# Kernel optimization log

Hardware: AMD Instinct MI355X
Metric: run time of the kernel (lower is better)

Reference implementation:

```python
import jax, jax.numpy as jnp
import numpy as np

B, T, D = 2, 4096, 1024
HD, HQ, KVH, W = 128, 8, 1, 1024   # head_dim, q_heads, kv_heads, window
HH, HG, K = 1536, 2048, 4          # hawk hidden, gmlp hidden, conv kernel
ALPHA_SCALE = float(np.log(8.0))   # alpha_log_scale (stored as log, used exp'd)


def setup_inputs() -> dict:
    key = jax.random.key(0)
    ks = jax.random.split(key, 16)
    n = lambda k, shape, std: jax.random.normal(k, shape, jnp.float32) * std
    return {
        'x': n(ks[0], (B, T, D), 1.0),
        'sn_g': jnp.ones((D,), jnp.float32),
        'q_w': n(ks[1], (HQ * HD, D), D ** -0.5),
        'kv_w': n(ks[2], (2 * KVH * HD, D), D ** -0.5),
        'ao_w': n(ks[3], (D, D), D ** -0.5),
        'sgn_g': jnp.ones((D,), jnp.float32),
        'sg_grow': n(ks[4], (2 * HG, D), D ** -0.5),
        'sg_shrink': n(ks[5], (D, HG), HG ** -0.5),
        'hn_g': jnp.ones((D,), jnp.float32),
        'h_in_w': n(ks[6], (2 * HH, D), D ** -0.5),
        'h_conv_w': n(ks[7], (HH, 1, K), K ** -0.5),
        'h_conv_b': jnp.zeros((HH,), jnp.float32),
        'h_gates_w': n(ks[8], (2 * HH, HH), HH ** -0.5),
        'h_gates_b': jnp.zeros((2 * HH,), jnp.float32),
        'h_forget': jnp.linspace(-4.323, -9.0, HH, dtype=jnp.float32),
        'h_out_w': n(ks[9], (D, HH), HH ** -0.5),
        'hgn_g': jnp.ones((D,), jnp.float32),
        'hg_grow': n(ks[10], (2 * HG, D), D ** -0.5),
        'hg_shrink': n(ks[11], (D, HG), HG ** -0.5),
    }


def rmsnorm(x, gamma):
    # original: gamma / dim**-0.5 * x / ||x||_2  (no eps)
    inv = jax.lax.rsqrt(jnp.sum(x * x, axis=-1, keepdims=True))
    return gamma * (x.shape[-1] ** 0.5) * x * inv


def rope(x, base=10000.0):
    # x: (B, T, H, HD); interleaved rotary over time axis 1
    t = x.shape[1]
    hd = x.shape[-1]
    inv = 1.0 / (base ** (jnp.arange(0, hd, 2, dtype=jnp.float32) / hd))
    ang = jnp.arange(t, dtype=jnp.float32)[:, None] * inv[None, :]  # (T, HD/2)
    cos = jnp.cos(ang)[None, :, None, :]
    sin = jnp.sin(ang)[None, :, None, :]
    x1, x2 = x[..., 0::2], x[..., 1::2]
    y1 = x1 * cos - x2 * sin
    y2 = x1 * sin + x2 * cos
    return jnp.stack([y1, y2], axis=-1).reshape(x.shape)


def sliding_mqa(x, q_w, kv_w, ao_w):
    # MQA with causal sliding window of W, computed in blocks of W
    q = (x @ q_w.T).reshape(B, T, HQ, HD)
    kv = (x @ kv_w.T).reshape(B, T, 2, KVH, HD)
    k = kv[:, :, 0, 0]  # (B, T, HD) since KVH == 1
    v = kv[:, :, 1, 0]
    q = rope(q)
    k = rope(k[:, :, None, :])[:, :, 0]
    nb = T // W
    qb = q.reshape(B, nb, W, HQ, HD)
    kb = k.reshape(B, nb, W, HD)
    vb = v.reshape(B, nb, W, HD)
    # prepend previous block (zeros for block 0)
    shift = lambda a: jnp.concatenate([jnp.zeros_like(a[:, :1]), a[:, :-1]], axis=1)
    k2 = jnp.concatenate([shift(kb), kb], axis=2)  # (B, nb, 2W, HD)
    v2 = jnp.concatenate([shift(vb), vb], axis=2)
    qi = jnp.arange(W)[:, None]
    kj = jnp.arange(2 * W)[None, :]
    base = (kj >= qi) & (kj <= qi + W)  # causal + window (i-j <= W)
    blk0 = base & (kj >= W)             # block 0 has no real previous block
    mask = jnp.where(jnp.arange(nb)[:, None, None] == 0, blk0[None], base[None])
    scores = jnp.einsum('bnqhd,bnkd->bhnqk', qb, k2) * (HD ** -0.5)
    scores = jnp.where(mask[None, None], scores, -jnp.inf)
    p = jax.nn.softmax(scores, axis=-1)
    o = jnp.einsum('bhnqk,bnkd->bnqhd', p, v2).reshape(B, T, HQ * HD)
    return o @ ao_w.T


def gated_mlp(x, grow_w, shrink_w):
    gate, h = jnp.split(x @ grow_w.T, 2, axis=-1)
    return (jax.nn.gelu(gate, approximate=False) * h) @ shrink_w.T


def hawk(x, in_w, conv_w, conv_b, gates_w, gates_b, forget_base, out_w):
    gate, u = jnp.split(x @ in_w.T, 2, axis=-1)  # (B, T, HH) each
    # depthwise causal conv1d (torch pads k-1 both sides then slices [:T])
    u_nch = jnp.transpose(u, (0, 2, 1))  # (B, HH, T)
    c = jax.lax.conv_general_dilated(
        u_nch, conv_w, window_strides=(1,), padding=[(K - 1, 0)],
        feature_group_count=HH, dimension_numbers=('NCH', 'OIH', 'NCH'))
    xc = jnp.transpose(c + conv_b[None, :, None], (0, 2, 1))  # (B, T, HH)
    fg, ig = jnp.split(xc @ gates_w.T + gates_b, 2, axis=-1)
    log_alpha = -np.exp(ALPHA_SCALE) * jax.nn.softplus(forget_base) * jax.nn.sigmoid(fg)
    alpha = jnp.exp(log_alpha)
    beta = jnp.sqrt(1.0 - alpha * alpha + 1e-6)
    xin = beta * jax.nn.sigmoid(ig) * xc
    # linear recurrence h_t = alpha_t * h_{t-1} + xin_t  via associative scan
    def combine(c1, c2):
        a1, x1 = c1
        a2, x2 = c2
        return a1 * a2, a2 * x1 + x2
    _, h = jax.lax.associative_scan(combine, (alpha, xin), axis=1)
    return (jax.nn.gelu(gate, approximate=False) * h) @ out_w.T


def reference(x, sn_g, q_w, kv_w, ao_w, sgn_g, sg_grow, sg_shrink,
              hn_g, h_in_w, h_conv_w, h_conv_b, h_gates_w, h_gates_b,
              h_forget, h_out_w, hgn_g, hg_grow, hg_shrink):
    x = x + sliding_mqa(rmsnorm(x, sn_g), q_w, kv_w, ao_w)
    x = x + gated_mlp(rmsnorm(x, sgn_g), sg_grow, sg_shrink)
    x = x + hawk(rmsnorm(x, hn_g), h_in_w, h_conv_w, h_conv_b,
                 h_gates_w, h_gates_b, h_forget, h_out_w)
    x = x + gated_mlp(rmsnorm(x, hgn_g), hg_grow, hg_shrink)
    return x
```

## Files before the change

### kernel.cpp

```cpp
#include <hip/hip_runtime.h>
#include <hip/hip_bf16.h>
#include <math.h>

#define B_  2
#define T_  4096
#define D_  1024
#define HD_ 128
#define HQ_ 8
#define W_  1024
#define HH_ 1536
#define HG_ 2048
#define KC_ 4

typedef float  f32x4  __attribute__((ext_vector_type(4)));
typedef float  f32x2  __attribute__((ext_vector_type(2)));
typedef __bf16 bf16x8 __attribute__((ext_vector_type(8)));
typedef unsigned short u16;
typedef unsigned short u16x2 __attribute__((ext_vector_type(2)));
typedef unsigned short u16x4 __attribute__((ext_vector_type(4)));
typedef unsigned short u16x8 __attribute__((ext_vector_type(8)));

__device__ __forceinline__ u16 f2bf(float f) {
    unsigned int u = __builtin_bit_cast(unsigned int, f);
    u += 0x7fffu + ((u >> 16) & 1u);
    return (u16)(u >> 16);
}
__device__ __forceinline__ float bf2f(u16 v) {
    unsigned int u = ((unsigned int)v) << 16;
    return __builtin_bit_cast(float, u);
}
__device__ __forceinline__ float gelu_exact(float x) {
    return 0.5f * x * (1.0f + erff(x * 0.70710678118654752f));
}
__device__ __forceinline__ float sigmoidf_(float x) {
    return 1.0f / (1.0f + expf(-x));
}

#define GLOAD16(gp, lp) __builtin_amdgcn_global_load_lds( \
    (const __attribute__((address_space(1))) void*)(gp),  \
    (__attribute__((address_space(3))) void*)(lp), 16, 0, 0)

struct CvtArgs {
    const float* src[10];
    u16* dst[10];
    long cum[11];
};
__global__ __launch_bounds__(256)
void cvt_all_kernel(CvtArgs a)
{
    long i = ((long)blockIdx.x * 256 + threadIdx.x) * 8;
    if (i >= a.cum[10]) return;
    int seg = 0;
#pragma unroll
    for (int s = 1; s < 10; s++) if (i >= a.cum[s]) seg = s;
    long off = i - a.cum[seg];
    const float* src = a.src[seg];
    u16* dst = a.dst[seg];
    f32x4 x = *(const f32x4*)(src + off);
    f32x4 y = *(const f32x4*)(src + off + 4);
    u16x4 ua, ub;
    ua.x = f2bf(x.x); ua.y = f2bf(x.y); ua.z = f2bf(x.z); ua.w = f2bf(x.w);
    ub.x = f2bf(y.x); ub.y = f2bf(y.y); ub.z = f2bf(y.z); ub.w = f2bf(y.w);
    *(u16x4*)(dst + off) = ua;
    *(u16x4*)(dst + off + 4) = ub;
}

template<int EPI, bool OBF>
__global__ __launch_bounds__(512)
void gemm_big64_kernel(const u16* __restrict__ A, const u16* __restrict__ Bw,
                       const float* __restrict__ bias, const float* __restrict__ res,
                       const u16* gatebuf, void* outv,
                       int M, int N, int K)
{
    __shared__ u16 lA[3][256 * 64];
    __shared__ u16 lB[3][128 * 64];
    const int n0 = blockIdx.x * 128, m0 = blockIdx.y * 256;
    const int tid = threadIdx.x, w = tid >> 6, l = tid & 63;
    const int wr = w >> 1, wc = w & 1;
    const int lr = l & 15, lg = l >> 4;

    f32x4 acc[4][4];
#pragma unroll
    for (int i = 0; i < 4; i++)
#pragma unroll
        for (int j = 0; j < 4; j++) acc[i][j] = {0.f, 0.f, 0.f, 0.f};

    const int srow = tid >> 3;
    const int gslot = (tid & 7) ^ ((tid >> 3) & 7);
    const u16* gA = A + (long)(m0 + srow) * K + gslot * 8;
    const u16* gB = Bw + (long)(n0 + srow) * K + gslot * 8;
    const int lofs = tid * 8;

#define STAGE_G(buf, kk)                                              \
    {                                                                 \
        GLOAD16(gA + (kk),                 &lA[buf][lofs]);           \
        GLOAD16(gA + (long)64 * K + (kk),  &lA[buf][4096 + lofs]);    \
        GLOAD16(gA + (long)128 * K + (kk), &lA[buf][8192 + lofs]);    \
        GLOAD16(gA + (long)192 * K + (kk), &lA[buf][12288 + lofs]);   \
        GLOAD16(gB + (kk),                 &lB[buf][lofs]);           \
        GLOAD16(gB + (long)64 * K + (kk),  &lB[buf][4096 + lofs]);    \
    }

    const int NT = K >> 6;
    STAGE_G(0, 0);
    STAGE_G(1, 64);

    const int swz = lr & 7;
    int cur = 0;
    for (int t = 0; t < NT; ++t) {
        if (t == NT - 1) { asm volatile("s_waitcnt vmcnt(0)" ::: "memory"); }
        else             { asm volatile("s_waitcnt vmcnt(6)" ::: "memory"); }
        __builtin_amdgcn_s_barrier();
        __builtin_amdgcn_sched_barrier(0);
        if (t + 2 < NT) {
            int nb = cur + 2; if (nb >= 3) nb -= 3;
            STAGE_G(nb, (t + 2) << 6);
        }
#pragma unroll
        for (int ks = 0; ks < 2; ks++) {
            bf16x8 af[4], bfr[4];
#pragma unroll
            for (int m = 0; m < 4; m++)
                af[m] = *(const bf16x8*)&lA[cur][(wr * 64 + m * 16 + lr) * 64 + (((ks * 4 + lg) ^ swz) * 8)];
#pragma unroll
            for (int n = 0; n < 4; n++)
                bfr[n] = *(const bf16x8*)&lB[cur][(wc * 64 + n * 16 + lr) * 64 + (((ks * 4 + lg) ^ swz) * 8)];
            __builtin_amdgcn_s_setprio(1);
#pragma unroll
            for (int m = 0; m < 4; m++)
#pragma unroll
                for (int n = 0; n < 4; n++)
                    acc[m][n] = __builtin_amdgcn_mfma_f32_16x16x32_bf16(af[m], bfr[n], acc[m][n], 0, 0, 0);
            __builtin_amdgcn_s_setprio(0);
        }
        cur++; if (cur == 3) cur = 0;
    }
#undef STAGE_G

#pragma unroll
    for (int m = 0; m < 4; m++)
#pragma unroll
        for (int n = 0; n < 4; n++) {
            const int col = n0 + wc * 64 + n * 16 + lr;
            const float bv = (EPI == 1) ? bias[col] : 0.f;
#pragma unroll
            for (int r = 0; r < 4; r++) {
                const int row = m0 + wr * 64 + m * 16 + lg * 4 + r;
                const long idx = (long)row * N + col;
                float v = acc[m][n][r] + bv;
                if (EPI == 2) v += res[idx];
                if (EPI == 3) v = gelu_exact(bf2f(gatebuf[idx])) * v;
                if (OBF) ((u16*)outv)[idx] = f2bf(v);
                else     ((float*)outv)[idx] = v;
            }
        }
}

template<int EPI, bool OBF>
__global__ __launch_bounds__(256)
void gemm_bf16_kernel(const u16* __restrict__ A, const u16* __restrict__ Bw,
                      const float* __restrict__ bias, const float* __restrict__ res,
                      const u16* gatebuf, void* outv,
                      int M, int N, int K)
{
    __shared__ u16 lA[3][128 * 32];
    __shared__ u16 lB[3][128 * 32];
    const int n0 = blockIdx.x * 128, m0 = blockIdx.y * 128;
    const int tid = threadIdx.x, w = tid >> 6, l = tid & 63;
    const int wr = w >> 1, wc = w & 1, lr = l & 15, lg = l >> 4;

    f32x4 acc[4][4];
#pragma unroll
    for (int i = 0; i < 4; i++)
#pragma unroll
        for (int j = 0; j < 4; j++) acc[i][j] = {0.f, 0.f, 0.f, 0.f};

    const int srow = w * 16 + (l >> 2);
    const int gslot = ((l & 3) - ((l >> 3) & 3)) & 3;
    const u16* gA = A + (long)(m0 + srow) * K + gslot * 8;
    const u16* gB = Bw + (long)(n0 + srow) * K + gslot * 8;
    const int lofs = w * 512 + l * 8;

#define STAGE_G(buf, kk)                                          \
    {                                                             \
        GLOAD16(gA + (kk),                &lA[buf][lofs]);        \
        GLOAD16(gA + (long)64 * K + (kk), &lA[buf][2048 + lofs]); \
        GLOAD16(gB + (kk),                &lB[buf][lofs]);        \
        GLOAD16(gB + (long)64 * K + (kk), &lB[buf][2048 + lofs]); \
    }

    const int NT = K >> 5;
    STAGE_G(0, 0);
    STAGE_G(1, 32);

    const int swzr = (lr >> 1) & 3;
    int cur = 0;
    for (int t = 0; t < NT; ++t) {
        if (t == NT - 1) { asm volatile("s_waitcnt vmcnt(0)" ::: "memory"); }
        else             { asm volatile("s_waitcnt vmcnt(4)" ::: "memory"); }
        __builtin_amdgcn_s_barrier();
        __builtin_amdgcn_sched_barrier(0);
        if (t + 2 < NT) {
            int nb = cur + 2; if (nb >= 3) nb -= 3;
            STAGE_G(nb, (t + 2) << 5);
        }
        bf16x8 af[4], bfr[4];
#pragma unroll
        for (int m = 0; m < 4; m++)
            af[m] = *(const bf16x8*)&lA[cur][(wr * 64 + m * 16 + lr) * 32 + (((lg + swzr) & 3) * 8)];
#pragma unroll
        for (int n = 0; n < 4; n++)
            bfr[n] = *(const bf16x8*)&lB[cur][(wc * 64 + n * 16 + lr) * 32 + (((lg + swzr) & 3) * 8)];
        __builtin_amdgcn_s_setprio(1);
#pragma unroll
        for (int m = 0; m < 4; m++)
#pragma unroll
            for (int n = 0; n < 4; n++)
                acc[m][n] = __builtin_amdgcn_mfma_f32_16x16x32_bf16(af[m], bfr[n], acc[m][n], 0, 0, 0);
        __builtin_amdgcn_s_setprio(0);
        cur++; if (cur == 3) cur = 0;
    }
#undef STAGE_G

#pragma unroll
    for (int m = 0; m < 4; m++)
#pragma unroll
        for (int n = 0; n < 4; n++) {
            const int col = n0 + wc * 64 + n * 16 + lr;
            const float bv = (EPI == 1) ? bias[col] : 0.f;
#pragma unroll
            for (int r = 0; r < 4; r++) {
                const int row = m0 + wr * 64 + m * 16 + lg * 4 + r;
                const long idx = (long)row * N + col;
                float v = acc[m][n][r] + bv;
                if (EPI == 2) v += res[idx];
                if (EPI == 3) v = gelu_exact(bf2f(gatebuf[idx])) * v;
                if (OBF) ((u16*)outv)[idx] = f2bf(v);
                else     ((float*)outv)[idx] = v;
            }
        }
}

__global__ __launch_bounds__(256)
void rmsnorm_kernel(const float* __restrict__ x, const float* __restrict__ g,
                    u16* __restrict__ out)
{
    const long row = blockIdx.x;
    const int tid = threadIdx.x;
    const float* xp = x + row * D_;
    f32x4 v = *(const f32x4*)(xp + tid * 4);
    float ss = v.x * v.x + v.y * v.y + v.z * v.z + v.w * v.w;
#pragma unroll
    for (int o = 1; o < 64; o <<= 1) ss += __shfl_xor(ss, o);
    __shared__ float ps[4];
    if ((tid & 63) == 0) ps[tid >> 6] = ss;
    __syncthreads();
    float tot = ps[0] + ps[1] + ps[2] + ps[3];
    float inv = rsqrtf(tot) * 32.0f;
    f32x4 gv = *(const f32x4*)(g + tid * 4);
    u16x4 o4;
    o4.x = f2bf(gv.x * v.x * inv); o4.y = f2bf(gv.y * v.y * inv);
    o4.z = f2bf(gv.z * v.z * inv); o4.w = f2bf(gv.w * v.w * inv);
    *(u16x4*)(out + row * D_ + tid * 4) = o4;
}

__global__ void rope_bf16_kernel(const float* __restrict__ q, const float* __restrict__ kv,
                                 u16* __restrict__ qb, u16* __restrict__ kb)
{
    const long NQ = (long)B_ * T_ * HQ_ * 64;
    const long NK = (long)B_ * T_ * 64;
    long idx = (long)blockIdx.x * blockDim.x + threadIdx.x;
    if (idx >= NQ + NK) return;
    int i; long t; const float* src; u16* dst;
    if (idx < NQ) {
        i = idx & 63;
        long bth = idx >> 6;
        t = (bth / HQ_) % T_;
        src = q + bth * HD_ + 2 * i;
        dst = qb + bth * HD_ + 2 * i;
    } else {
        long k = idx - NQ;
        i = k & 63;
        long bt = k >> 6;
        t = bt % T_;
        src = kv + bt * (2 * HD_) + 2 * i;
        dst = kb + bt * HD_ + 2 * i;
    }
    float freq = exp2f(-(float)i * 0.20762050593046014f);
    float ang = (float)t * freq;
    float sn, cs;
    sincosf(ang, &sn, &cs);
    f32x2 xv = *(const f32x2*)src;
    u16x2 yv;
    yv.x = f2bf(xv.x * cs - xv.y * sn);
    yv.y = f2bf(xv.x * sn + xv.y * cs);
    *(u16x2*)dst = yv;
}

__global__ __launch_bounds__(256)
void vtrans_kernel(const float* __restrict__ kv, u16* __restrict__ vt)
{
    __shared__ float tile[64][65];
    const int t0 = blockIdx.x * 64, d0 = blockIdx.y * 64, b = blockIdx.z;
    const int tid = threadIdx.x;
    {
        const int tl = tid & 63, dg = tid >> 6;
        const float* vp = kv + (((long)b * T_ + t0 + tl) * 2 + 1) * HD_ + d0 + dg * 16;
#pragma unroll
        for (int j = 0; j < 4; j++) {
            f32x4 v = *(const f32x4*)(vp + j * 4);
            tile[dg * 16 + j * 4 + 0][tl] = v.x;
            tile[dg * 16 + j * 4 + 1][tl] = v.y;
            tile[dg * 16 + j * 4 + 2][tl] = v.z;
            tile[dg * 16 + j * 4 + 3][tl] = v.w;
        }
    }
    __syncthreads();
    {
        const int dl = tid >> 2, tg = (tid & 3) * 16;
        u16x8 a, c;
#pragma unroll
        for (int j = 0; j < 8; j++) a[j] = f2bf(tile[dl][tg + j]);
#pragma unroll
        for (int j = 0; j < 8; j++) c[j] = f2bf(tile[dl][tg + 8 + j]);
        u16* dst = vt + ((long)b * HD_ + d0 + dl) * T_ + t0 + tg;
        *(u16x8*)dst = a;
        *(u16x8*)(dst + 8) = c;
    }
}

#define PLD 72

__global__ __launch_bounds__(256)
void attn_mfma3_kernel(const u16* __restrict__ qb, const u16* __restrict__ kb,
                       const u16* __restrict__ vt, u16* __restrict__ o)
{
    __shared__ u16 Ksh[2][64 * 128];
    __shared__ u16 Vsh[2][128 * 64];
    __shared__ u16 Psh[4 * 16 * PLD];

    const int qt = blockIdx.x, h = blockIdx.y, b = blockIdx.z;
    const int q0 = qt * 64;
    const int tid = threadIdx.x;
    const int w = tid >> 6, l = tid & 63;
    const int lr = l & 15, lg = l >> 4;

    bf16x8 qfr[4];
    {
        const u16* qp = qb + (((long)b * T_ + q0 + w * 16 + lr) * HQ_ + h) * HD_;
#pragma unroll
        for (int kt = 0; kt < 4; kt++)
            qfr[kt] = *(const bf16x8*)(qp + kt * 32 + lg * 8);
    }

    int oK[4], oV[4];
#pragma unroll
    for (int i = 0; i < 4; i++) {
        int krow = w * 16 + i * 4 + (l >> 4);
        int kc8 = (l & 15) ^ (krow & 7);
        oK[i] = krow * 128 + kc8 * 8;
        int vrow = w * 32 + i * 8 + (l >> 3);
        int vc8 = (l & 7) ^ (vrow & 7);
        oV[i] = vrow * T_ + vc8 * 8;
    }
    const u16* kbase = kb + (long)b * T_ * HD_;
    const u16* vbase = vt + (long)b * HD_ * T_;

    f32x4 oacc[8];
#pragma unroll
    for (int dt = 0; dt < 8; dt++) oacc[dt] = {0.f, 0.f, 0.f, 0.f};
    float mrun[4], srun[4];
#pragma unroll
    for (int r = 0; r < 4; r++) { mrun[r] = -1e30f; srun[r] = 0.f; }

    const int kt_lo = (q0 >= W_) ? (q0 - W_) : 0;
    const int nt = ((q0 - kt_lo) >> 6) + 1;
    const int sw = lr & 7;
    const float scale = 0.08838834764831845f;

#pragma unroll
    for (int i = 0; i < 4; i++) {
        GLOAD16(kbase + (long)kt_lo * HD_ + oK[i], &Ksh[0][w * 2048 + i * 512]);
        GLOAD16(vbase + kt_lo + oV[i], &Vsh[0][w * 2048 + i * 512]);
    }

    for (int t = 0; t < nt; ++t) {
        const int kt0 = kt_lo + t * 64;
        const int cur = t & 1;
        if (t + 1 < nt) {
            const int ktn = kt0 + 64;
#pragma unroll
            for (int i = 0; i < 4; i++) {
                GLOAD16(kbase + (long)ktn * HD_ + oK[i], &Ksh[cur ^ 1][w * 2048 + i * 512]);
                GLOAD16(vbase + ktn + oV[i], &Vsh[cur ^ 1][w * 2048 + i * 512]);
            }
            asm volatile("s_waitcnt vmcnt(8)" ::: "memory");
        } else {
            asm volatile("s_waitcnt vmcnt(0)" ::: "memory");
        }
        __builtin_amdgcn_s_barrier();
        __builtin_amdgcn_sched_barrier(0);

        const u16* Kc = Ksh[cur];
        const u16* Vc = Vsh[cur];

        f32x4 s[4];
        __builtin_amdgcn_s_setprio(1);
#pragma unroll
        for (int ct = 0; ct < 4; ct++) {
            s[ct] = {0.f, 0.f, 0.f, 0.f};
#pragma unroll
            for (int kt = 0; kt < 4; kt++) {
                bf16x8 kf = *(const bf16x8*)&Kc[(ct * 16 + lr) * 128 + (((kt * 4 + lg) ^ sw) * 8)];
                s[ct] = __builtin_amdgcn_mfma_f32_16x16x32_bf16(qfr[kt], kf, s[ct], 0, 0, 0);
            }
        }
        __builtin_amdgcn_s_setprio(0);

        float tmax[4] = {-3e38f, -3e38f, -3e38f, -3e38f};
        if (kt0 == q0) {
#pragma unroll
            for (int ct = 0; ct < 4; ct++) {
                const int kpos = kt0 + ct * 16 + lr;
#pragma unroll
                for (int r = 0; r < 4; r++) {
                    const int qpos = q0 + w * 16 + lg * 4 + r;
                    float v = s[ct][r] * scale;
                    v = (kpos <= qpos) ? v : -3e38f;
                    s[ct][r] = v;
                    tmax[r] = fmaxf(tmax[r], v);
                }
            }
        } else if (kt0 == q0 - W_) {
#pragma unroll
            for (int ct = 0; ct < 4; ct++) {
                const int kpos = kt0 + ct * 16 + lr;
#pragma unroll
                for (int r = 0; r < 4; r++) {
                    const int qpos = q0 + w * 16 + lg * 4 + r;
                    float v = s[ct][r] * scale;
                    v = (kpos + W_ >= qpos) ? v : -3e38f;
                    s[ct][r] = v;
                    tmax[r] = fmaxf(tmax[r], v);
                }
            }
        } else {
#pragma unroll
            for (int ct = 0; ct < 4; ct++)
#pragma unroll
                for (int r = 0; r < 4; r++) {
                    float v = s[ct][r] * scale;
                    s[ct][r] = v;
                    tmax[r] = fmaxf(tmax[r], v);
                }
        }
#pragma unroll
        for (int r = 0; r < 4; r++)
#pragma unroll
            for (int msk = 1; msk < 16; msk <<= 1)
                tmax[r] = fmaxf(tmax[r], __shfl_xor(tmax[r], msk));

        bool defer = (tmax[0] <= mrun[0] + 8.f) && (tmax[1] <= mrun[1] + 8.f) &&
                     (tmax[2] <= mrun[2] + 8.f) && (tmax[3] <= mrun[3] + 8.f);
        if (!__all(defer)) {
            float frv[4];
#pragma unroll
            for (int r = 0; r < 4; r++) {
                float mnew = fmaxf(mrun[r], tmax[r]);
                frv[r] = __expf(mrun[r] - mnew);
                mrun[r] = mnew;
                srun[r] *= frv[r];
            }
#pragma unroll
            for (int dt = 0; dt < 8; dt++) {
                oacc[dt][0] *= frv[0]; oacc[dt][1] *= frv[1];
                oacc[dt][2] *= frv[2]; oacc[dt][3] *= frv[3];
            }
        }

        u16* pw = &Psh[w * 16 * PLD];
        float psum[4] = {0.f, 0.f, 0.f, 0.f};
#pragma unroll
        for (int ct = 0; ct < 4; ct++)
#pragma unroll
            for (int r = 0; r < 4; r++) {
                float p = __expf(s[ct][r] - mrun[r]);
                psum[r] += p;
                pw[(lg * 4 + r) * PLD + ct * 16 + lr] = f2bf(p);
            }
#pragma unroll
        for (int r = 0; r < 4; r++) {
#pragma unroll
            for (int msk = 1; msk < 16; msk <<= 1)
                psum[r] += __shfl_xor(psum[r], msk);
            srun[r] += psum[r];
        }

        asm volatile("s_waitcnt lgkmcnt(0)" ::: "memory");
        bf16x8 pa0 = *(const bf16x8*)&pw[lr * PLD + lg * 8];
        bf16x8 pa1 = *(const bf16x8*)&pw[lr * PLD + 32 + lg * 8];
        __builtin_amdgcn_s_setprio(1);
#pragma unroll
        for (int dt = 0; dt < 8; dt++) {
            bf16x8 vf0 = *(const bf16x8*)&Vc[(dt * 16 + lr) * 64 + ((lg ^ sw) * 8)];
            bf16x8 vf1 = *(const bf16x8*)&Vc[(dt * 16 + lr) * 64 + (((4 + lg) ^ sw) * 8)];
            oacc[dt] = __builtin_amdgcn_mfma_f32_16x16x32_bf16(pa0, vf0, oacc[dt], 0, 0, 0);
            oacc[dt] = __builtin_amdgcn_mfma_f32_16x16x32_bf16(pa1, vf1, oacc[dt], 0, 0, 0);
        }
        __builtin_amdgcn_s_setprio(0);
        __syncthreads();
    }

#pragma unroll
    for (int r = 0; r < 4; r++) {
        const int qpos = q0 + w * 16 + lg * 4 + r;
        float inv = 1.f / srun[r];
        u16* op = o + ((long)b * T_ + qpos) * (HQ_ * HD_) + h * HD_;
#pragma unroll
        for (int dt = 0; dt < 8; dt++)
            op[dt * 16 + lr] = f2bf(oacc[dt][r] * inv);
    }
}

__global__ void conv_kernel(const u16* __restrict__ u, const float* __restrict__ w,
                            const float* __restrict__ bias, u16* __restrict__ xc)
{
    long idx = (long)blockIdx.x * blockDim.x + threadIdx.x;
    if (idx >= (long)B_ * T_ * HH_) return;
    int ch = (int)(idx % HH_);
    long row = idx / HH_;
    int t = (int)(row % T_);
    float acc = bias[ch];
#pragma unroll
    for (int k = 0; k < KC_; k++) {
        int ts = t - 3 + k;
        if (ts >= 0) acc += bf2f(u[(row - t + ts) * HH_ + ch]) * w[ch * KC_ + k];
    }
    xc[idx] = f2bf(acc);
}

#define CS_ 64
#define NC_ (T_ / CS_)

__device__ __forceinline__ void alpha_xin(const u16 fg, const u16 ig, const u16 xc,
                                          float sp, float& a, float& xin)
{
    a = expf(-8.0f * sp * sigmoidf_(bf2f(fg)));
    xin = sqrtf(1.f - a * a + 1e-6f) * sigmoidf_(bf2f(ig)) * bf2f(xc);
}

__global__ void scan1_kernel(const u16* __restrict__ fg, const u16* __restrict__ ig,
                             const u16* __restrict__ xc, const float* __restrict__ fb,
                             float* __restrict__ P, float* __restrict__ L)
{
    long idx = (long)blockIdx.x * blockDim.x + threadIdx.x;
    if (idx >= (long)B_ * NC_ * HH_) return;
    int ch = (int)(idx % HH_);
    int chunk = (int)((idx / HH_) % NC_);
    int b = (int)(idx / ((long)HH_ * NC_));
    long base = ((long)b * T_ + chunk * CS_) * HH_ + ch;
    float f = fb[ch];
    float sp = (f > 20.f) ? f : log1pf(expf(f));
    float p = 1.f, lacc = 0.f;
    for (int i = 0; i < CS_; i++) {
        long o = base + (long)i * HH_;
        float a, xin;
        alpha_xin(fg[o], ig[o], xc[o], sp, a, xin);
        lacc = a * lacc + xin;
        p *= a;
    }
    P[idx] = p; L[idx] = lacc;
}
__global__ void scan2_kernel(const float* __restrict__ P, const float* __restrict__ L,
                             float* __restrict__ I)
{
    long idx = (long)blockIdx.x * blockDim.x + threadIdx.x;
    if (idx >= (long)B_ * HH_) return;
    int ch = (int)(idx % HH_);
    int b = (int)(idx / HH_);
    float init = 0.f;
    for (int c = 0; c < NC_; c++) {
        long o = ((long)b * NC_ + c) * HH_ + ch;
        I[o] = init;
        init = P[o] * init + L[o];
    }
}
__global__ void scan3_kernel(const u16* __restrict__ fg, const u16* __restrict__ ig,
                             const u16* __restrict__ xc, const float* __restrict__ fb,
                             const float* __restrict__ I, const u16* __restrict__ gate,
                             u16* __restrict__ glu)
{
    long idx = (long)blockIdx.x * blockDim.x + threadIdx.x;
    if (idx >= (long)B_ * NC_ * HH_) return;
    int ch = (int)(idx % HH_);
    int chunk = (int)((idx / HH_) % NC_);
    int b = (int)(idx / ((long)HH_ * NC_));
    long base = ((long)b * T_ + chunk * CS_) * HH_ + ch;
    float f = fb[ch];
    float sp = (f > 20.f) ? f : log1pf(expf(f));
    float h = I[idx];
    for (int i = 0; i < CS_; i++) {
        long o = base + (long)i * HH_;
        float a, xin;
        alpha_xin(fg[o], ig[o], xc[o], sp, a, xin);
        h = a * h + xin;
        glu[o] = f2bf(gelu_exact(bf2f(gate[o])) * h);
    }
}

static inline long cdivl(long a, long b) { return (a + b - 1) / b; }

extern "C" void kernel_launch(void* const* d_in, const int* in_sizes, int n_in,
                              void* d_out, int out_size, void* d_ws, size_t ws_size,
                              hipStream_t stream)
{
    const float* x_in   = (const float*)d_in[0];
    const float* sn_g   = (const float*)d_in[1];
    const float* q_w    = (const float*)d_in[2];
    const float* kv_w   = (const float*)d_in[3];
    const float* ao_w   = (const float*)d_in[4];
    const float* sgn_g  = (const float*)d_in[5];
    const float* sg_grow   = (const float*)d_in[6];
    const float* sg_shrink = (const float*)d_in[7];
    const float* hn_g   = (const float*)d_in[8];
    const float* h_in_w = (const float*)d_in[9];
    const float* h_conv_w = (const float*)d_in[10];
    const float* h_conv_b = (const float*)d_in[11];
    const float* h_gates_w = (const float*)d_in[12];
    const float* h_gates_b = (const float*)d_in[13];
    const float* h_forget  = (const float*)d_in[14];
    const float* h_out_w   = (const float*)d_in[15];
    const float* hgn_g  = (const float*)d_in[16];
    const float* hg_grow   = (const float*)d_in[17];
    const float* hg_shrink = (const float*)d_in[18];
    float* out = (float*)d_out;

    char* wsb = (char*)d_ws;
    u16* Wq  = (u16*)wsb;
    u16* Wkv = Wq  + 1048576;
    u16* Wao = Wkv + 262144;
    u16* Wsg = Wao + 1048576;
    u16* Wss = Wsg + 4194304;
    u16* Whi = Wss + 2097152;
    u16* Whg = Whi + 3145728;
    u16* Who = Whg + 4718592;
    u16* Wgg = Who + 1572864;
    u16* Wgs = Wgg + 4194304;
    char* ab = wsb + 48758784;
    u16*   XN   = (u16*)(ab + 0);
    char*  S2   = ab + 16777216;
    char*  S3   = ab + 50331648;
    char*  S4   = ab + 75497472;
    char*  S5   = ab + 100663296;
    char*  S6   = ab + 125829120;
    float* PB   = (float*)(ab + 150994944);
    float* LB   = (float*)(ab + 151781376);
    float* IB   = (float*)(ab + 152567808);

    const long M = (long)B_ * T_;
    dim3 blk(256);
    dim3 blk5(512);
    const float* NULF = nullptr;
    const u16*   NULB = nullptr;

    {
        CvtArgs ca;
        const float* srcs[10] = {q_w, kv_w, ao_w, sg_grow, sg_shrink,
                                 h_in_w, h_gates_w, h_out_w, hg_grow, hg_shrink};
        u16* dsts[10] = {Wq, Wkv, Wao, Wsg, Wss, Whi, Whg, Who, Wgg, Wgs};
        long ns[10] = {1048576, 262144, 1048576, 4194304, 2097152,
                       3145728, 4718592, 1572864, 4194304, 2097152};
        long cum = 0;
        for (int i = 0; i < 10; i++) {
            ca.src[i] = srcs[i]; ca.dst[i] = dsts[i]; ca.cum[i] = cum; cum += ns[i];
        }
        ca.cum[10] = cum;
        cvt_all_kernel<<<dim3(cdivl(cum / 8, 256)), blk, 0, stream>>>(ca);
    }

    {
        float* Q  = (float*)S2;
        float* KV = (float*)S3;
        u16*   Kb = (u16*)(S3 + 8388608);
        u16*   Vt = (u16*)(S3 + 10485760);
        u16*   Qb = (u16*)S4;
        u16*   AT = (u16*)S5;
        rmsnorm_kernel<<<dim3(M), blk, 0, stream>>>(x_in, sn_g, XN);
        gemm_big64_kernel<0,false><<<dim3(8, 32), blk5, 0, stream>>>(XN, Wq, NULF, NULF, NULB, Q, M, 1024, 1024);
        gemm_bf16_kernel<0,false><<<dim3(2, 64), blk, 0, stream>>>(XN, Wkv, NULF, NULF, NULB, KV, M, 256, 1024);
        rope_bf16_kernel<<<dim3(cdivl((long)B_ * T_ * (HQ_ + 1) * 64, 256)), blk, 0, stream>>>(Q, KV, Qb, Kb);
        vtrans_kernel<<<dim3(T_ / 64, 2, B_), blk, 0, stream>>>(KV, Vt);
        attn_mfma3_kernel<<<dim3(T_ / 64, HQ_, B_), blk, 0, stream>>>(Qb, Kb, Vt, AT);
        gemm_big64_kernel<2,false><<<dim3(8, 32), blk5, 0, stream>>>(AT, Wao, NULF, x_in, NULB, out, M, 1024, 1024);
    }

    {
        u16* GATE = (u16*)S2;
        rmsnorm_kernel<<<dim3(M), blk, 0, stream>>>(out, sgn_g, XN);
        gemm_big64_kernel<0,true><<<dim3(16, 32), blk5, 0, stream>>>(XN, Wsg, NULF, NULF, NULB, GATE, M, 2048, 1024);
        gemm_big64_kernel<3,true><<<dim3(16, 32), blk5, 0, stream>>>(XN, Wsg + (size_t)2048 * 1024, NULF, NULF, GATE, GATE, M, 2048, 1024);
        gemm_big64_kernel<2,false><<<dim3(8, 32), blk5, 0, stream>>>(GATE, Wss, NULF, out, NULB, out, M, 1024, 2048);
    }

    {
        u16* GATEH = (u16*)S2;
        u16* U     = (u16*)S3;
        u16* XC    = (u16*)S4;
        u16* FG    = (u16*)S5;
        u16* IG    = (u16*)S6;
        rmsnorm_kernel<<<dim3(M), blk, 0, stream>>>(out, hn_g, XN);
        gemm_bf16_kernel<0,true><<<dim3(12, 64), blk, 0, stream>>>(XN, Whi, NULF, NULF, NULB, GATEH, M, 1536, 1024);
        gemm_bf16_kernel<0,true><<<dim3(12, 64), blk, 0, stream>>>(XN, Whi + (size_t)1536 * 1024, NULF, NULF, NULB, U, M, 1536, 1024);
        conv_kernel<<<dim3(cdivl(M * HH_, 256)), blk, 0, stream>>>(U, h_conv_w, h_conv_b, XC);
        gemm_bf16_kernel<1,true><<<dim3(12, 64), blk, 0, stream>>>(XC, Whg, h_gates_b, NULF, NULB, FG, M, 1536, 1536);
        gemm_bf16_kernel<1,true><<<dim3(12, 64), blk, 0, stream>>>(XC, Whg + (size_t)1536 * 1536, h_gates_b + 1536, NULF, NULB, IG, M, 1536, 1536);
        scan1_kernel<<<dim3(cdivl((long)B_ * NC_ * HH_, 256)), blk, 0, stream>>>(FG, IG, XC, h_forget, PB, LB);
        scan2_kernel<<<dim3(cdivl((long)B_ * HH_, 256)), blk, 0, stream>>>(PB, LB, IB);
        scan3_kernel<<<dim3(cdivl((long)B_ * NC_ * HH_, 256)), blk, 0, stream>>>(FG, IG, XC, h_forget, IB, GATEH, U);
        gemm_big64_kernel<2,false><<<dim3(8, 32), blk5, 0, stream>>>(U, Who, NULF, out, NULB, out, M, 1024, 1536);
    }

    {
        u16* GLU = (u16*)S2;
        rmsnorm_kernel<<<dim3(M), blk, 0, stream>>>(out, hgn_g, XN);
        gemm_big64_kernel<0,true><<<dim3(16, 32), blk5, 0, stream>>>(XN, Wgg, NULF, NULF, NULB, GLU, M, 2048, 1024);
        gemm_big64_kernel<3,true><<<dim3(16, 32), blk5, 0, stream>>>(XN, Wgg + (size_t)2048 * 1024, NULF, NULF, GLU, GLU, M, 2048, 1024);
        gemm_big64_kernel<2,false><<<dim3(8, 32), blk5, 0, stream>>>(GLU, Wgs, NULF, out, NULB, out, M, 1024, 2048);
    }
}
```

Baseline: 1.085 ms.

## Restructure big GEMM main loop into phased LDS-read/MFMA/prefetch interleave

```diff
diff --git a/kernel.cpp b/kernel.cpp
--- a/kernel.cpp
+++ b/kernel.cpp
@@ -67,10 +67,10 @@
 
 template<int EPI, bool OBF>
 __global__ __launch_bounds__(512)
-void gemm_big64_kernel(const u16* __restrict__ A, const u16* __restrict__ Bw,
-                       const float* __restrict__ bias, const float* __restrict__ res,
-                       const u16* gatebuf, void* outv,
-                       int M, int N, int K)
+void gemm_8ph_kernel(const u16* __restrict__ A, const u16* __restrict__ Bw,
+                     const float* __restrict__ bias, const float* __restrict__ res,
+                     const u16* gatebuf, void* outv,
+                     int M, int N, int K)
 {
     __shared__ u16 lA[3][256 * 64];
     __shared__ u16 lB[3][128 * 64];
@@ -91,51 +91,113 @@
     const u16* gB = Bw + (long)(n0 + srow) * K + gslot * 8;
     const int lofs = tid * 8;
 
-#define STAGE_G(buf, kk)                                              \
-    {                                                                 \
-        GLOAD16(gA + (kk),                 &lA[buf][lofs]);           \
-        GLOAD16(gA + (long)64 * K + (kk),  &lA[buf][4096 + lofs]);    \
-        GLOAD16(gA + (long)128 * K + (kk), &lA[buf][8192 + lofs]);    \
-        GLOAD16(gA + (long)192 * K + (kk), &lA[buf][12288 + lofs]);   \
-        GLOAD16(gB + (kk),                 &lB[buf][lofs]);           \
-        GLOAD16(gB + (long)64 * K + (kk),  &lB[buf][4096 + lofs]);    \
-    }
+#define SG_A0(buf, kk) { GLOAD16(gA + (kk),                 &lA[buf][lofs]);         \
+                         GLOAD16(gA + (long)64 * K + (kk),  &lA[buf][4096 + lofs]); }
+#define SG_A1(buf, kk) { GLOAD16(gA + (long)128 * K + (kk), &lA[buf][8192 + lofs]);  \
+                         GLOAD16(gA + (long)192 * K + (kk), &lA[buf][12288 + lofs]); }
+#define SG_B(buf, kk)  { GLOAD16(gB + (kk),                 &lB[buf][lofs]);         \
+                         GLOAD16(gB + (long)64 * K + (kk),  &lB[buf][4096 + lofs]); }
 
     const int NT = K >> 6;
-    STAGE_G(0, 0);
-    STAGE_G(1, 64);
+    SG_A0(0, 0); SG_A1(0, 0); SG_B(0, 0);
+    SG_A0(1, 64); SG_A1(1, 64); SG_B(1, 64);
+    asm volatile("s_waitcnt vmcnt(6)" ::: "memory");
+    __builtin_amdgcn_s_barrier();
 
     const int swz = lr & 7;
+#define RD_A(buf, m, ks) (*(const bf16x8*)&lA[buf][(wr * 64 + (m) * 16 + lr) * 64 + ((((ks) * 4 + lg) ^ swz) * 8)])
+#define RD_B(buf, n, ks) (*(const bf16x8*)&lB[buf][(wc * 64 + (n) * 16 + lr) * 64 + ((((ks) * 4 + lg) ^ swz) * 8)])
+
     int cur = 0;
     for (int t = 0; t < NT; ++t) {
-        if (t == NT - 1) { asm volatile("s_waitcnt vmcnt(0)" ::: "memory"); }
-        else             { asm volatile("s_waitcnt vmcnt(6)" ::: "memory"); }
-        __builtin_amdgcn_s_barrier();
+        int nb = cur + 2; if (nb >= 3) nb -= 3;
+        const bool pf = (t + 2 < NT);
+        const int kk2 = (t + 2) << 6;
+        bf16x8 fa[2][2], fb0[2][2], fb2[2][2];
+
+#pragma unroll
+        for (int m = 0; m < 2; m++)
+#pragma unroll
+            for (int ks = 0; ks < 2; ks++) fa[m][ks] = RD_A(cur, m, ks);
+#pragma unroll
+        for (int n = 0; n < 2; n++)
+#pragma unroll
+            for (int ks = 0; ks < 2; ks++) fb0[n][ks] = RD_B(cur, n, ks);
+        if (pf) SG_A0(nb, kk2);
+        __builtin_amdgcn_s_barrier();
+        asm volatile("s_waitcnt lgkmcnt(0)" ::: "memory");
         __builtin_amdgcn_sched_barrier(0);
-        if (t + 2 < NT) {
-            int nb = cur + 2; if (nb >= 3) nb -= 3;
-            STAGE_G(nb, (t + 2) << 6);
-        }
-#pragma unroll
-        for (int ks = 0; ks < 2; ks++) {
-            bf16x8 af[4], bfr[4];
-#pragma unroll
-            for (int m = 0; m < 4; m++)
-                af[m] = *(const bf16x8*)&lA[cur][(wr * 64 + m * 16 + lr) * 64 + (((ks * 4 + lg) ^ swz) * 8)];
-#pragma unroll
-            for (int n = 0; n < 4; n++)
-                bfr[n] = *(const bf16x8*)&lB[cur][(wc * 64 + n * 16 + lr) * 64 + (((ks * 4 + lg) ^ swz) * 8)];
-            __builtin_amdgcn_s_setprio(1);
-#pragma unroll
-            for (int m = 0; m < 4; m++)
-#pragma unroll
-                for (int n = 0; n < 4; n++)
-                    acc[m][n] = __builtin_amdgcn_mfma_f32_16x16x32_bf16(af[m], bfr[n], acc[m][n], 0, 0, 0);
-            __builtin_amdgcn_s_setprio(0);
-        }
+        __builtin_amdgcn_s_setprio(1);
+#pragma unroll
+        for (int m = 0; m < 2; m++)
+#pragma unroll
+            for (int n = 0; n < 2; n++)
+#pragma unroll
+                for (int ks = 0; ks < 2; ks++)
+                    acc[m][n] = __builtin_amdgcn_mfma_f32_16x16x32_bf16(fa[m][ks], fb0[n][ks], acc[m][n], 0, 0, 0);
+        __builtin_amdgcn_s_setprio(0);
+        __builtin_amdgcn_s_barrier();
+
+#pragma unroll
+        for (int n = 0; n < 2; n++)
+#pragma unroll
+            for (int ks = 0; ks < 2; ks++) fb2[n][ks] = RD_B(cur, n + 2, ks);
+        if (pf) SG_A1(nb, kk2);
+        __builtin_amdgcn_s_barrier();
+        asm volatile("s_waitcnt lgkmcnt(0)" ::: "memory");
+        __builtin_amdgcn_sched_barrier(0);
+        __builtin_amdgcn_s_setprio(1);
+#pragma unroll
+        for (int m = 0; m < 2; m++)
+#pragma unroll
+            for (int n = 0; n < 2; n++)
+#pragma unroll
+                for (int ks = 0; ks < 2; ks++)
+                    acc[m][n + 2] = __builtin_amdgcn_mfma_f32_16x16x32_bf16(fa[m][ks], fb2[n][ks], acc[m][n + 2], 0, 0, 0);
+        __builtin_amdgcn_s_setprio(0);
+        __builtin_amdgcn_s_barrier();
+
+#pragma unroll
+        for (int m = 0; m < 2; m++)
+#pragma unroll
+            for (int ks = 0; ks < 2; ks++) fa[m][ks] = RD_A(cur, m + 2, ks);
+        if (pf) SG_B(nb, kk2);
+        __builtin_amdgcn_s_barrier();
+        asm volatile("s_waitcnt lgkmcnt(0)" ::: "memory");
+        __builtin_amdgcn_sched_barrier(0);
+        __builtin_amdgcn_s_setprio(1);
+#pragma unroll
+        for (int m = 0; m < 2; m++)
+#pragma unroll
+            for (int n = 0; n < 2; n++)
+#pragma unroll
+                for (int ks = 0; ks < 2; ks++)
+                    acc[m + 2][n + 2] = __builtin_amdgcn_mfma_f32_16x16x32_bf16(fa[m][ks], fb2[n][ks], acc[m + 2][n + 2], 0, 0, 0);
+        __builtin_amdgcn_s_setprio(0);
+        __builtin_amdgcn_s_barrier();
+
+        if (t + 1 < NT) { asm volatile("s_waitcnt vmcnt(6)" ::: "memory"); }
+        else            { asm volatile("s_waitcnt vmcnt(0)" ::: "memory"); }
+        __builtin_amdgcn_s_barrier();
+        __builtin_amdgcn_sched_barrier(0);
+        __builtin_amdgcn_s_setprio(1);
+#pragma unroll
+        for (int m = 0; m < 2; m++)
+#pragma unroll
+            for (int n = 0; n < 2; n++)
+#pragma unroll
+                for (int ks = 0; ks < 2; ks++)
+                    acc[m + 2][n] = __builtin_amdgcn_mfma_f32_16x16x32_bf16(fa[m][ks], fb0[n][ks], acc[m + 2][n], 0, 0, 0);
+        __builtin_amdgcn_s_setprio(0);
+        __builtin_amdgcn_s_barrier();
+
         cur++; if (cur == 3) cur = 0;
     }
-#undef STAGE_G
+#undef SG_A0
+#undef SG_A1
+#undef SG_B
+#undef RD_A
+#undef RD_B
 
 #pragma unroll
     for (int m = 0; m < 4; m++)
@@ -686,20 +748,20 @@
         u16*   Qb = (u16*)S4;
         u16*   AT = (u16*)S5;
         rmsnorm_kernel<<<dim3(M), blk, 0, stream>>>(x_in, sn_g, XN);
-        gemm_big64_kernel<0,false><<<dim3(8, 32), blk5, 0, stream>>>(XN, Wq, NULF, NULF, NULB, Q, M, 1024, 1024);
+        gemm_8ph_kernel<0,false><<<dim3(8, 32), blk5, 0, stream>>>(XN, Wq, NULF, NULF, NULB, Q, M, 1024, 1024);
         gemm_bf16_kernel<0,false><<<dim3(2, 64), blk, 0, stream>>>(XN, Wkv, NULF, NULF, NULB, KV, M, 256, 1024);
         rope_bf16_kernel<<<dim3(cdivl((long)B_ * T_ * (HQ_ + 1) * 64, 256)), blk, 0, stream>>>(Q, KV, Qb, Kb);
         vtrans_kernel<<<dim3(T_ / 64, 2, B_), blk, 0, stream>>>(KV, Vt);
         attn_mfma3_kernel<<<dim3(T_ / 64, HQ_, B_), blk, 0, stream>>>(Qb, Kb, Vt, AT);
-        gemm_big64_kernel<2,false><<<dim3(8, 32), blk5, 0, stream>>>(AT, Wao, NULF, x_in, NULB, out, M, 1024, 1024);
+        gemm_8ph_kernel<2,false><<<dim3(8, 32), blk5, 0, stream>>>(AT, Wao, NULF, x_in, NULB, out, M, 1024, 1024);
     }
 
     {
         u16* GATE = (u16*)S2;
         rmsnorm_kernel<<<dim3(M), blk, 0, stream>>>(out, sgn_g, XN);
-        gemm_big64_kernel<0,true><<<dim3(16, 32), blk5, 0, stream>>>(XN, Wsg, NULF, NULF, NULB, GATE, M, 2048, 1024);
-        gemm_big64_kernel<3,true><<<dim3(16, 32), blk5, 0, stream>>>(XN, Wsg + (size_t)2048 * 1024, NULF, NULF, GATE, GATE, M, 2048, 1024);
-        gemm_big64_kernel<2,false><<<dim3(8, 32), blk5, 0, stream>>>(GATE, Wss, NULF, out, NULB, out, M, 1024, 2048);
+        gemm_8ph_kernel<0,true><<<dim3(16, 32), blk5, 0, stream>>>(XN, Wsg, NULF, NULF, NULB, GATE, M, 2048, 1024);
+        gemm_8ph_kernel<3,true><<<dim3(16, 32), blk5, 0, stream>>>(XN, Wsg + (size_t)2048 * 1024, NULF, NULF, GATE, GATE, M, 2048, 1024);
+        gemm_8ph_kernel<2,false><<<dim3(8, 32), blk5, 0, stream>>>(GATE, Wss, NULF, out, NULB, out, M, 1024, 2048);
     }
 
     {
@@ -717,14 +779,14 @@
         scan1_kernel<<<dim3(cdivl((long)B_ * NC_ * HH_, 256)), blk, 0, stream>>>(FG, IG, XC, h_forget, PB, LB);
         scan2_kernel<<<dim3(cdivl((long)B_ * HH_, 256)), blk, 0, stream>>>(PB, LB, IB);
         scan3_kernel<<<dim3(cdivl((long)B_ * NC_ * HH_, 256)), blk, 0, stream>>>(FG, IG, XC, h_forget, IB, GATEH, U);
-        gemm_big64_kernel<2,false><<<dim3(8, 32), blk5, 0, stream>>>(U, Who, NULF, out, NULB, out, M, 1024, 1536);
+        gemm_8ph_kernel<2,false><<<dim3(8, 32), blk5, 0, stream>>>(U, Who, NULF, out, NULB, out, M, 1024, 1536);
     }
 
     {
         u16* GLU = (u16*)S2;
         rmsnorm_kernel<<<dim3(M), blk, 0, stream>>>(out, hgn_g, XN);
-        gemm_big64_kernel<0,true><<<dim3(16, 32), blk5, 0, stream>>>(XN, Wgg, NULF, NULF, NULB, GLU, M, 2048, 1024);
-        gemm_big64_kernel<3,true><<<dim3(16, 32), blk5, 0, stream>>>(XN, Wgg + (size_t)2048 * 1024, NULF, NULF, GLU, GLU, M, 2048, 1024);
-        gemm_big64_kernel<2,false><<<dim3(8, 32), blk5, 0, stream>>>(GLU, Wgs, NULF, out, NULB, out, M, 1024, 2048);
-    }
-}
+        gemm_8ph_kernel<0,true><<<dim3(16, 32), blk5, 0, stream>>>(XN, Wgg, NULF, NULF, NULB, GLU, M, 2048, 1024);
+        gemm_8ph_kernel<3,true><<<dim3(16, 32), blk5, 0, stream>>>(XN, Wgg + (size_t)2048 * 1024, NULF, NULF, GLU, GLU, M, 2048, 1024);
+        gemm_8ph_kernel<2,false><<<dim3(8, 32), blk5, 0, stream>>>(GLU, Wgs, NULF, out, NULB, out, M, 1024, 2048);
+    }
+}
```

Measured after the change: 1.053 ms. 1.03x faster.
